# Kernel tuning notes

Measured on AMD Instinct MI355X. Metric: run time of the kernel, lower is better.

## Reference

```python
import jax, jax.numpy as jnp
import numpy as np

WORLD_SIZE = 8
BS = 16
MSG = 16384


def setup_inputs() -> dict:
    key = jax.random.key(0)
    k0, k1, kw, kb = jax.random.split(key, 4)
    x0 = jax.random.normal(k0, (WORLD_SIZE, BS, MSG), dtype=jnp.float32)
    x1 = jax.random.normal(k1, (WORLD_SIZE, BS, MSG), dtype=jnp.float32)
    # nn.Linear(msg_size, msg_size) params, kaiming-uniform-ish scale
    scale = 1.0 / np.sqrt(MSG)
    W = jax.random.uniform(kw, (MSG, MSG), dtype=jnp.float32, minval=-scale, maxval=scale)
    b = jax.random.uniform(kb, (MSG,), dtype=jnp.float32, minval=-scale, maxval=scale)
    return {"x0": x0, "x1": x1, "W": W, "b": b}


def reference(x0, x1, W, b):
    # all_gather_ll: concat per-rank shards along dim 0 -> [world_size*bs, msg]
    t0 = x0.reshape(WORLD_SIZE * BS, MSG)
    t1 = x1.reshape(WORLD_SIZE * BS, MSG)
    # shared Linear applied to both gathered tensors: y = t @ W^T + b
    y0 = jnp.einsum("nk,mk->nm", t0, W) + b
    y1 = jnp.einsum("nk,mk->nm", t1, W) + b
    return (y0, y1)
```

## Files before the change

### kernel.cpp

```cpp
#include <hip/hip_runtime.h>
#include <hip/hip_bf16.h>

typedef __bf16 bf16x8 __attribute__((ext_vector_type(8)));
typedef float  f32x4  __attribute__((ext_vector_type(4)));

#define N_TOT   16384
#define K_TOT   16384
#define HALF_M  ((size_t)128 * 16384)
#define BN      128
#define BK      32
#define KSPLIT  4
#define KQ_LEN  (K_TOT / KSPLIT)
#define NQSTEPS (KQ_LEN / BK)
#define OUT_ELEMS ((size_t)256 * 16384)

__device__ __forceinline__ unsigned short f2bf(float f) {
    __hip_bfloat16 h = __float2bfloat16(f);
    return __builtin_bit_cast(unsigned short, h);
}

__device__ __forceinline__ int swz64(int row, int g) {
    return row * 64 + (((g ^ ((row >> 1) & 3)) & 3) << 4);
}

__global__ void cvtT_kernel(const float* __restrict__ x0,
                            const float* __restrict__ x1,
                            unsigned short* __restrict__ wsT) {
    size_t i = (size_t)blockIdx.x * blockDim.x + threadIdx.x;
    size_t e = i * 8;
    const float* src = (e < HALF_M) ? (x0 + e) : (x1 + (e - HALF_M));
    float4 a = ((const float4*)src)[0];
    float4 b = ((const float4*)src)[1];
    union { unsigned short u[8]; uint4 v; } o;
    o.u[0] = f2bf(a.x); o.u[1] = f2bf(a.y); o.u[2] = f2bf(a.z); o.u[3] = f2bf(a.w);
    o.u[4] = f2bf(b.x); o.u[5] = f2bf(b.y); o.u[6] = f2bf(b.z); o.u[7] = f2bf(b.w);
    ((uint4*)wsT)[i] = o.v;
}

__global__ void combine_kernel(float* __restrict__ out,
                               const float* __restrict__ p0,
                               const float* __restrict__ p1,
                               const float* __restrict__ p2) {
    const size_t n4 = OUT_ELEMS / 4;
    size_t i = (size_t)blockIdx.x * blockDim.x + threadIdx.x;
    for (; i < n4; i += (size_t)gridDim.x * blockDim.x) {
        float4 o = ((const float4*)out)[i];
        float4 a = ((const float4*)p0)[i];
        float4 b = ((const float4*)p1)[i];
        float4 c = ((const float4*)p2)[i];
        o.x += a.x + b.x + c.x;  o.y += a.y + b.y + c.y;
        o.z += a.z + b.z + c.z;  o.w += a.w + b.w + c.w;
        ((float4*)out)[i] = o;
    }
}

#define ISSUEW(S, k0) do {                                                    \
    const uint4* _p = (const uint4*)(arow_w + (k0));                          \
    w##S##_0 = _p[0]; w##S##_1 = _p[1];                                       \
    const float4* _q = (const float4*)(brow + (k0));                          \
    wb##S##_0 = _q[0]; wb##S##_1 = _q[1];                                     \
} while (0)

#define STAGEW(S, Ab, Bb) do {                                                \
    *(uint4*)((Ab) + aw0) = w##S##_0;                                         \
    *(uint4*)((Ab) + aw1) = w##S##_1;                                         \
    union { unsigned short u[8]; uint4 v; } _tb;                              \
    _tb.u[0]=f2bf(wb##S##_0.x); _tb.u[1]=f2bf(wb##S##_0.y);                   \
    _tb.u[2]=f2bf(wb##S##_0.z); _tb.u[3]=f2bf(wb##S##_0.w);                   \
    _tb.u[4]=f2bf(wb##S##_1.x); _tb.u[5]=f2bf(wb##S##_1.y);                   \
    _tb.u[6]=f2bf(wb##S##_1.z); _tb.u[7]=f2bf(wb##S##_1.w);                   \
    *(uint4*)((Bb) + bw) = _tb.v;                                             \
} while (0)

#define COMPUTE(Ab, Bb) do {                                                  \
    bf16x8 _vb0 = *(const bf16x8*)((Bb) + boff0);                             \
    bf16x8 _vb1 = *(const bf16x8*)((Bb) + boff0 + 1024);                      \
    bf16x8 _va;                                                               \
    _va = *(const bf16x8*)((Ab) + aoff0 + 0*1024);                            \
    accA0 = __builtin_amdgcn_mfma_f32_16x16x32_bf16(_va, _vb0, accA0, 0,0,0); \
    accB0 = __builtin_amdgcn_mfma_f32_16x16x32_bf16(_va, _vb1, accB0, 0,0,0); \
    _va = *(const bf16x8*)((Ab) + aoff0 + 1*1024);                            \
    accA1 = __builtin_amdgcn_mfma_f32_16x16x32_bf16(_va, _vb0, accA1, 0,0,0); \
    accB1 = __builtin_amdgcn_mfma_f32_16x16x32_bf16(_va, _vb1, accB1, 0,0,0); \
    _va = *(const bf16x8*)((Ab) + aoff0 + 2*1024);                            \
    accA2 = __builtin_amdgcn_mfma_f32_16x16x32_bf16(_va, _vb0, accA2, 0,0,0); \
    accB2 = __builtin_amdgcn_mfma_f32_16x16x32_bf16(_va, _vb1, accB2, 0,0,0); \
    _va = *(const bf16x8*)((Ab) + aoff0 + 3*1024);                            \
    accA3 = __builtin_amdgcn_mfma_f32_16x16x32_bf16(_va, _vb0, accA3, 0,0,0); \
    accB3 = __builtin_amdgcn_mfma_f32_16x16x32_bf16(_va, _vb1, accB3, 0,0,0); \
    _va = *(const bf16x8*)((Ab) + aoff0 + 4*1024);                            \
    accA4 = __builtin_amdgcn_mfma_f32_16x16x32_bf16(_va, _vb0, accA4, 0,0,0); \
    accB4 = __builtin_amdgcn_mfma_f32_16x16x32_bf16(_va, _vb1, accB4, 0,0,0); \
    _va = *(const bf16x8*)((Ab) + aoff0 + 5*1024);                            \
    accA5 = __builtin_amdgcn_mfma_f32_16x16x32_bf16(_va, _vb0, accA5, 0,0,0); \
    accB5 = __builtin_amdgcn_mfma_f32_16x16x32_bf16(_va, _vb1, accB5, 0,0,0); \
    _va = *(const bf16x8*)((Ab) + aoff0 + 6*1024);                            \
    accA6 = __builtin_amdgcn_mfma_f32_16x16x32_bf16(_va, _vb0, accA6, 0,0,0); \
    accB6 = __builtin_amdgcn_mfma_f32_16x16x32_bf16(_va, _vb1, accB6, 0,0,0); \
    _va = *(const bf16x8*)((Ab) + aoff0 + 7*1024);                            \
    accA7 = __builtin_amdgcn_mfma_f32_16x16x32_bf16(_va, _vb0, accA7, 0,0,0); \
    accB7 = __builtin_amdgcn_mfma_f32_16x16x32_bf16(_va, _vb1, accB7, 0,0,0); \
} while (0)

#define SYNC do {                                                             \
    asm volatile("s_waitcnt lgkmcnt(0)" ::: "memory");                        \
    __builtin_amdgcn_s_barrier();                                             \
    __builtin_amdgcn_sched_barrier(0);                                        \
} while (0)

__global__ __launch_bounds__(512, 4)
void gemm_ws(const float* __restrict__ W, const float* __restrict__ bias,
             const unsigned short* __restrict__ wsT,
             float* __restrict__ out, float* __restrict__ wsP)
{
    __shared__ uint4 smem_[(2 * 16384 + 2 * 8192) / 16];
    char* const sm = (char*)smem_;
    char* const A0 = sm;
    char* const A1 = sm + 16384;
    char* const B0 = sm + 32768;
    char* const B1 = sm + 32768 + 8192;

    const int tid  = threadIdx.x;
    const int lane = tid & 63;
    const int wave = tid >> 6;
    const int wm = wave >> 2;
    const int wn = wave & 3;
    const int bid    = blockIdx.x;
    const int kq     = bid >> 7;
    const int nstrip = bid & 127;
    const int n0     = nstrip * BN;
    const int kbase  = kq * KQ_LEN;

    const int ra = tid >> 1;
    const int pa = tid & 1;
    const int rb = tid >> 2;
    const int gb = tid & 3;

    const unsigned short* arow_w = wsT + (size_t)ra * K_TOT + kbase + pa * 16;
    const float* brow = W + (size_t)(n0 + rb) * K_TOT + kbase + gb * 8;

    const int aw0 = swz64(ra, 2 * pa);
    const int aw1 = swz64(ra, 2 * pa + 1);
    const int bw  = swz64(rb, gb);

    const int aoff0 = swz64(wm * 128 + (lane & 15), lane >> 4);
    const int boff0 = swz64(wn * 32 + (lane & 15), lane >> 4);

    f32x4 accA0={0.f,0.f,0.f,0.f}, accA1={0.f,0.f,0.f,0.f};
    f32x4 accA2={0.f,0.f,0.f,0.f}, accA3={0.f,0.f,0.f,0.f};
    f32x4 accA4={0.f,0.f,0.f,0.f}, accA5={0.f,0.f,0.f,0.f};
    f32x4 accA6={0.f,0.f,0.f,0.f}, accA7={0.f,0.f,0.f,0.f};
    f32x4 accB0={0.f,0.f,0.f,0.f}, accB1={0.f,0.f,0.f,0.f};
    f32x4 accB2={0.f,0.f,0.f,0.f}, accB3={0.f,0.f,0.f,0.f};
    f32x4 accB4={0.f,0.f,0.f,0.f}, accB5={0.f,0.f,0.f,0.f};
    f32x4 accB6={0.f,0.f,0.f,0.f}, accB7={0.f,0.f,0.f,0.f};

    uint4  w0_0, w0_1, w1_0, w1_1;
    float4 wb0_0, wb0_1, wb1_0, wb1_1;

    ISSUEW(0, 0);
    ISSUEW(1, BK);
    STAGEW(0, A0, B0);
    SYNC;

    for (int kt = 0; kt < NQSTEPS; kt += 2) {
        if (kt + 2 < NQSTEPS) ISSUEW(0, (kt + 2) * BK);
        COMPUTE(A0, B0);
        STAGEW(1, A1, B1);
        SYNC;
        if (kt + 3 < NQSTEPS) ISSUEW(1, (kt + 3) * BK);
        COMPUTE(A1, B1);
        if (kt + 2 < NQSTEPS) STAGEW(0, A0, B0);
        SYNC;
    }

    float* const dst = (kq == 0) ? out : (wsP + (size_t)(kq - 1) * OUT_ELEMS);
    #pragma unroll
    for (int nf = 0; nf < 2; ++nf) {
        const int col = n0 + wn * 32 + nf * 16 + (lane & 15);
        const float bv = (kq == 0) ? bias[col] : 0.f;
        #pragma unroll
        for (int mf = 0; mf < 8; ++mf) {
            const f32x4 a = (nf == 0)
                ? (mf==0?accA0:mf==1?accA1:mf==2?accA2:mf==3?accA3:
                   mf==4?accA4:mf==5?accA5:mf==6?accA6:accA7)
                : (mf==0?accB0:mf==1?accB1:mf==2?accB2:mf==3?accB3:
                   mf==4?accB4:mf==5?accB5:mf==6?accB6:accB7);
            #pragma unroll
            for (int j = 0; j < 4; ++j) {
                int r = wm * 128 + mf * 16 + (lane >> 4) * 4 + j;
                float v = a[j] + bv;
                float* o = (r < 128) ? (dst + (size_t)r * N_TOT + col)
                                     : (dst + HALF_M + (size_t)(r - 128) * N_TOT + col);
                *o = v;
            }
        }
    }
}

extern "C" void kernel_launch(void* const* d_in, const int* in_sizes, int n_in,
                              void* d_out, int out_size, void* d_ws, size_t ws_size,
                              hipStream_t stream) {
    const float* x0 = (const float*)d_in[0];
    const float* x1 = (const float*)d_in[1];
    const float* W  = (const float*)d_in[2];
    const float* b  = (const float*)d_in[3];
    float* out = (float*)d_out;

    const size_t wsT_bytes = (size_t)256 * 16384 * sizeof(unsigned short);

    unsigned short* wsT = (unsigned short*)d_ws;
    float* wsP = (float*)((char*)d_ws + wsT_bytes);

    cvtT_kernel<<<2048, 256, 0, stream>>>(x0, x1, wsT);
    gemm_ws<<<512, 512, 0, stream>>>(W, b, wsT, out, wsP);
    combine_kernel<<<2048, 256, 0, stream>>>(out, wsP, wsP + OUT_ELEMS,
                                             wsP + 2 * OUT_ELEMS);
}
```

Baseline: 322.6 us.

## Load W fragments straight to registers and let each wave cover all 256 rows

The GEMM block shrinks from 512 to 256 threads. Each of the 4 waves now owns a 32-column N slice and all 256 activation rows, so it holds 32 accumulator tiles. W is no longer staged through LDS: each lane loads its own fp32 W fragment from global memory, converts it to bf16 in registers and feeds it directly to MFMA. Only the activation tile stays in double-buffered LDS. This removes the LDS writes, reads and bank traffic for W and halves the LDS footprint, at the cost of much higher register pressure and lower occupancy. W global loads are also less coalesced per lane, since each lane reads a 32-byte chunk from a different row.

```diff
diff --git a/kernel.cpp b/kernel.cpp
--- a/kernel.cpp
+++ b/kernel.cpp
@@ -54,52 +54,51 @@
     }
 }
 
-#define ISSUEW(S, k0) do {                                                    \
-    const uint4* _p = (const uint4*)(arow_w + (k0));                          \
-    w##S##_0 = _p[0]; w##S##_1 = _p[1];                                       \
-    const float4* _q = (const float4*)(brow + (k0));                          \
-    wb##S##_0 = _q[0]; wb##S##_1 = _q[1];                                     \
-} while (0)
-
-#define STAGEW(S, Ab, Bb) do {                                                \
-    *(uint4*)((Ab) + aw0) = w##S##_0;                                         \
-    *(uint4*)((Ab) + aw1) = w##S##_1;                                         \
-    union { unsigned short u[8]; uint4 v; } _tb;                              \
-    _tb.u[0]=f2bf(wb##S##_0.x); _tb.u[1]=f2bf(wb##S##_0.y);                   \
-    _tb.u[2]=f2bf(wb##S##_0.z); _tb.u[3]=f2bf(wb##S##_0.w);                   \
-    _tb.u[4]=f2bf(wb##S##_1.x); _tb.u[5]=f2bf(wb##S##_1.y);                   \
-    _tb.u[6]=f2bf(wb##S##_1.z); _tb.u[7]=f2bf(wb##S##_1.w);                   \
-    *(uint4*)((Bb) + bw) = _tb.v;                                             \
-} while (0)
-
-#define COMPUTE(Ab, Bb) do {                                                  \
-    bf16x8 _vb0 = *(const bf16x8*)((Bb) + boff0);                             \
-    bf16x8 _vb1 = *(const bf16x8*)((Bb) + boff0 + 1024);                      \
-    bf16x8 _va;                                                               \
-    _va = *(const bf16x8*)((Ab) + aoff0 + 0*1024);                            \
-    accA0 = __builtin_amdgcn_mfma_f32_16x16x32_bf16(_va, _vb0, accA0, 0,0,0); \
-    accB0 = __builtin_amdgcn_mfma_f32_16x16x32_bf16(_va, _vb1, accB0, 0,0,0); \
-    _va = *(const bf16x8*)((Ab) + aoff0 + 1*1024);                            \
-    accA1 = __builtin_amdgcn_mfma_f32_16x16x32_bf16(_va, _vb0, accA1, 0,0,0); \
-    accB1 = __builtin_amdgcn_mfma_f32_16x16x32_bf16(_va, _vb1, accB1, 0,0,0); \
-    _va = *(const bf16x8*)((Ab) + aoff0 + 2*1024);                            \
-    accA2 = __builtin_amdgcn_mfma_f32_16x16x32_bf16(_va, _vb0, accA2, 0,0,0); \
-    accB2 = __builtin_amdgcn_mfma_f32_16x16x32_bf16(_va, _vb1, accB2, 0,0,0); \
-    _va = *(const bf16x8*)((Ab) + aoff0 + 3*1024);                            \
-    accA3 = __builtin_amdgcn_mfma_f32_16x16x32_bf16(_va, _vb0, accA3, 0,0,0); \
-    accB3 = __builtin_amdgcn_mfma_f32_16x16x32_bf16(_va, _vb1, accB3, 0,0,0); \
-    _va = *(const bf16x8*)((Ab) + aoff0 + 4*1024);                            \
-    accA4 = __builtin_amdgcn_mfma_f32_16x16x32_bf16(_va, _vb0, accA4, 0,0,0); \
-    accB4 = __builtin_amdgcn_mfma_f32_16x16x32_bf16(_va, _vb1, accB4, 0,0,0); \
-    _va = *(const bf16x8*)((Ab) + aoff0 + 5*1024);                            \
-    accA5 = __builtin_amdgcn_mfma_f32_16x16x32_bf16(_va, _vb0, accA5, 0,0,0); \
-    accB5 = __builtin_amdgcn_mfma_f32_16x16x32_bf16(_va, _vb1, accB5, 0,0,0); \
-    _va = *(const bf16x8*)((Ab) + aoff0 + 6*1024);                            \
-    accA6 = __builtin_amdgcn_mfma_f32_16x16x32_bf16(_va, _vb0, accA6, 0,0,0); \
-    accB6 = __builtin_amdgcn_mfma_f32_16x16x32_bf16(_va, _vb1, accB6, 0,0,0); \
-    _va = *(const bf16x8*)((Ab) + aoff0 + 7*1024);                            \
-    accA7 = __builtin_amdgcn_mfma_f32_16x16x32_bf16(_va, _vb0, accA7, 0,0,0); \
-    accB7 = __builtin_amdgcn_mfma_f32_16x16x32_bf16(_va, _vb1, accB7, 0,0,0); \
+#define ISSUE_A(S, kt) do {                                                   \
+    const uint4* _p = (const uint4*)(arow + (size_t)(kt) * BK);               \
+    a##S##_0 = _p[0]; a##S##_1 = _p[1]; a##S##_2 = _p[2]; a##S##_3 = _p[3];   \
+} while (0)
+
+#define STAGE_A(S, Ab) do {                                                   \
+    *(uint4*)((Ab) + sw0) = a##S##_0;                                         \
+    *(uint4*)((Ab) + sw1) = a##S##_1;                                         \
+    *(uint4*)((Ab) + sw2) = a##S##_2;                                         \
+    *(uint4*)((Ab) + sw3) = a##S##_3;                                         \
+} while (0)
+
+#define ISSUE_W(S, kt) do {                                                   \
+    const float4* _q0 = (const float4*)(wrow0 + (size_t)(kt) * BK);           \
+    w##S##_a0 = _q0[0]; w##S##_a1 = _q0[1];                                   \
+    const float4* _q1 = (const float4*)(wrow1 + (size_t)(kt) * BK);           \
+    w##S##_b0 = _q1[0]; w##S##_b1 = _q1[1];                                   \
+} while (0)
+
+#define CVT_W(S) do {                                                         \
+    union { unsigned short u[8]; bf16x8 v; } _c0, _c1;                        \
+    _c0.u[0]=f2bf(w##S##_a0.x); _c0.u[1]=f2bf(w##S##_a0.y);                   \
+    _c0.u[2]=f2bf(w##S##_a0.z); _c0.u[3]=f2bf(w##S##_a0.w);                   \
+    _c0.u[4]=f2bf(w##S##_a1.x); _c0.u[5]=f2bf(w##S##_a1.y);                   \
+    _c0.u[6]=f2bf(w##S##_a1.z); _c0.u[7]=f2bf(w##S##_a1.w);                   \
+    _c1.u[0]=f2bf(w##S##_b0.x); _c1.u[1]=f2bf(w##S##_b0.y);                   \
+    _c1.u[2]=f2bf(w##S##_b0.z); _c1.u[3]=f2bf(w##S##_b0.w);                   \
+    _c1.u[4]=f2bf(w##S##_b1.x); _c1.u[5]=f2bf(w##S##_b1.y);                   \
+    _c1.u[6]=f2bf(w##S##_b1.z); _c1.u[7]=f2bf(w##S##_b1.w);                   \
+    _vb0 = _c0.v; _vb1 = _c1.v;                                               \
+} while (0)
+
+#define MROW(MF, Ab) do {                                                     \
+    bf16x8 _va = *(const bf16x8*)((Ab) + aoff0 + MF * 1024);                  \
+    accA##MF = __builtin_amdgcn_mfma_f32_16x16x32_bf16(_va, _vb0, accA##MF, 0,0,0); \
+    accB##MF = __builtin_amdgcn_mfma_f32_16x16x32_bf16(_va, _vb1, accB##MF, 0,0,0); \
+} while (0)
+
+#define COMPUTE(Ab, S) do {                                                   \
+    bf16x8 _vb0, _vb1;                                                        \
+    CVT_W(S);                                                                 \
+    MROW(0, Ab);  MROW(1, Ab);  MROW(2, Ab);  MROW(3, Ab);                    \
+    MROW(4, Ab);  MROW(5, Ab);  MROW(6, Ab);  MROW(7, Ab);                    \
+    MROW(8, Ab);  MROW(9, Ab);  MROW(10, Ab); MROW(11, Ab);                   \
+    MROW(12, Ab); MROW(13, Ab); MROW(14, Ab); MROW(15, Ab);                   \
 } while (0)
 
 #define SYNC do {                                                             \
@@ -108,87 +107,90 @@
     __builtin_amdgcn_sched_barrier(0);                                        \
 } while (0)
 
-__global__ __launch_bounds__(512, 4)
+__global__ __launch_bounds__(256)
 void gemm_ws(const float* __restrict__ W, const float* __restrict__ bias,
              const unsigned short* __restrict__ wsT,
              float* __restrict__ out, float* __restrict__ wsP)
 {
-    __shared__ uint4 smem_[(2 * 16384 + 2 * 8192) / 16];
+    __shared__ uint4 smem_[2 * 16384 / 16];
     char* const sm = (char*)smem_;
     char* const A0 = sm;
     char* const A1 = sm + 16384;
-    char* const B0 = sm + 32768;
-    char* const B1 = sm + 32768 + 8192;
 
     const int tid  = threadIdx.x;
     const int lane = tid & 63;
     const int wave = tid >> 6;
-    const int wm = wave >> 2;
-    const int wn = wave & 3;
     const int bid    = blockIdx.x;
     const int kq     = bid >> 7;
     const int nstrip = bid & 127;
     const int n0     = nstrip * BN;
     const int kbase  = kq * KQ_LEN;
 
-    const int ra = tid >> 1;
-    const int pa = tid & 1;
-    const int rb = tid >> 2;
-    const int gb = tid & 3;
-
-    const unsigned short* arow_w = wsT + (size_t)ra * K_TOT + kbase + pa * 16;
-    const float* brow = W + (size_t)(n0 + rb) * K_TOT + kbase + gb * 8;
-
-    const int aw0 = swz64(ra, 2 * pa);
-    const int aw1 = swz64(ra, 2 * pa + 1);
-    const int bw  = swz64(rb, gb);
-
-    const int aoff0 = swz64(wm * 128 + (lane & 15), lane >> 4);
-    const int boff0 = swz64(wn * 32 + (lane & 15), lane >> 4);
-
-    f32x4 accA0={0.f,0.f,0.f,0.f}, accA1={0.f,0.f,0.f,0.f};
-    f32x4 accA2={0.f,0.f,0.f,0.f}, accA3={0.f,0.f,0.f,0.f};
-    f32x4 accA4={0.f,0.f,0.f,0.f}, accA5={0.f,0.f,0.f,0.f};
-    f32x4 accA6={0.f,0.f,0.f,0.f}, accA7={0.f,0.f,0.f,0.f};
-    f32x4 accB0={0.f,0.f,0.f,0.f}, accB1={0.f,0.f,0.f,0.f};
-    f32x4 accB2={0.f,0.f,0.f,0.f}, accB3={0.f,0.f,0.f,0.f};
-    f32x4 accB4={0.f,0.f,0.f,0.f}, accB5={0.f,0.f,0.f,0.f};
-    f32x4 accB6={0.f,0.f,0.f,0.f}, accB7={0.f,0.f,0.f,0.f};
-
-    uint4  w0_0, w0_1, w1_0, w1_1;
-    float4 wb0_0, wb0_1, wb1_0, wb1_1;
-
-    ISSUEW(0, 0);
-    ISSUEW(1, BK);
-    STAGEW(0, A0, B0);
+    const unsigned short* arow = wsT + (size_t)tid * K_TOT + kbase;
+    const int sw0 = swz64(tid, 0);
+    const int sw1 = swz64(tid, 1);
+    const int sw2 = swz64(tid, 2);
+    const int sw3 = swz64(tid, 3);
+
+    const int nrow0 = n0 + wave * 32 + (lane & 15);
+    const float* wrow0 = W + (size_t)nrow0 * K_TOT + kbase + (lane >> 4) * 8;
+    const float* wrow1 = wrow0 + (size_t)16 * K_TOT;
+
+    const int aoff0 = swz64(lane & 15, lane >> 4);
+
+    f32x4 accA0={0,0,0,0}, accA1={0,0,0,0}, accA2={0,0,0,0}, accA3={0,0,0,0};
+    f32x4 accA4={0,0,0,0}, accA5={0,0,0,0}, accA6={0,0,0,0}, accA7={0,0,0,0};
+    f32x4 accA8={0,0,0,0}, accA9={0,0,0,0}, accA10={0,0,0,0}, accA11={0,0,0,0};
+    f32x4 accA12={0,0,0,0}, accA13={0,0,0,0}, accA14={0,0,0,0}, accA15={0,0,0,0};
+    f32x4 accB0={0,0,0,0}, accB1={0,0,0,0}, accB2={0,0,0,0}, accB3={0,0,0,0};
+    f32x4 accB4={0,0,0,0}, accB5={0,0,0,0}, accB6={0,0,0,0}, accB7={0,0,0,0};
+    f32x4 accB8={0,0,0,0}, accB9={0,0,0,0}, accB10={0,0,0,0}, accB11={0,0,0,0};
+    f32x4 accB12={0,0,0,0}, accB13={0,0,0,0}, accB14={0,0,0,0}, accB15={0,0,0,0};
+
+    uint4  a0_0, a0_1, a0_2, a0_3, a1_0, a1_1, a1_2, a1_3;
+    float4 w0_a0, w0_a1, w0_b0, w0_b1, w1_a0, w1_a1, w1_b0, w1_b1;
+
+    ISSUE_A(0, 0); ISSUE_W(0, 0);
+    ISSUE_A(1, 1); ISSUE_W(1, 1);
+    STAGE_A(0, A0);
     SYNC;
 
     for (int kt = 0; kt < NQSTEPS; kt += 2) {
-        if (kt + 2 < NQSTEPS) ISSUEW(0, (kt + 2) * BK);
-        COMPUTE(A0, B0);
-        STAGEW(1, A1, B1);
-        SYNC;
-        if (kt + 3 < NQSTEPS) ISSUEW(1, (kt + 3) * BK);
-        COMPUTE(A1, B1);
-        if (kt + 2 < NQSTEPS) STAGEW(0, A0, B0);
-        SYNC;
+        {
+            const bool more = (kt + 2 < NQSTEPS);
+            COMPUTE(A0, 0);
+            if (more) { ISSUE_W(0, kt + 2); ISSUE_A(0, kt + 2); }
+            STAGE_A(1, A1);
+            SYNC;
+        }
+        {
+            const bool more = (kt + 3 < NQSTEPS);
+            COMPUTE(A1, 1);
+            if (more) { ISSUE_W(1, kt + 3); ISSUE_A(1, kt + 3); }
+            if (kt + 2 < NQSTEPS) STAGE_A(0, A0);
+            SYNC;
+        }
     }
 
     float* const dst = (kq == 0) ? out : (wsP + (size_t)(kq - 1) * OUT_ELEMS);
     #pragma unroll
     for (int nf = 0; nf < 2; ++nf) {
-        const int col = n0 + wn * 32 + nf * 16 + (lane & 15);
+        const int col = n0 + wave * 32 + nf * 16 + (lane & 15);
         const float bv = (kq == 0) ? bias[col] : 0.f;
         #pragma unroll
-        for (int mf = 0; mf < 8; ++mf) {
+        for (int mf = 0; mf < 16; ++mf) {
             const f32x4 a = (nf == 0)
                 ? (mf==0?accA0:mf==1?accA1:mf==2?accA2:mf==3?accA3:
-                   mf==4?accA4:mf==5?accA5:mf==6?accA6:accA7)
+                   mf==4?accA4:mf==5?accA5:mf==6?accA6:mf==7?accA7:
+                   mf==8?accA8:mf==9?accA9:mf==10?accA10:mf==11?accA11:
+                   mf==12?accA12:mf==13?accA13:mf==14?accA14:accA15)
                 : (mf==0?accB0:mf==1?accB1:mf==2?accB2:mf==3?accB3:
-                   mf==4?accB4:mf==5?accB5:mf==6?accB6:accB7);
+                   mf==4?accB4:mf==5?accB5:mf==6?accB6:mf==7?accB7:
+                   mf==8?accB8:mf==9?accB9:mf==10?accB10:mf==11?accB11:
+                   mf==12?accB12:mf==13?accB13:mf==14?accB14:accB15);
             #pragma unroll
             for (int j = 0; j < 4; ++j) {
-                int r = wm * 128 + mf * 16 + (lane >> 4) * 4 + j;
+                int r = mf * 16 + (lane >> 4) * 4 + j;
                 float v = a[j] + bv;
                 float* o = (r < 128) ? (dst + (size_t)r * N_TOT + col)
                                      : (dst + HALF_M + (size_t)(r - 128) * N_TOT + col);
@@ -213,7 +215,7 @@
     float* wsP = (float*)((char*)d_ws + wsT_bytes);
 
     cvtT_kernel<<<2048, 256, 0, stream>>>(x0, x1, wsT);
-    gemm_ws<<<512, 512, 0, stream>>>(W, b, wsT, out, wsP);
+    gemm_ws<<<512, 256, 0, stream>>>(W, b, wsT, out, wsP);
     combine_kernel<<<2048, 256, 0, stream>>>(out, wsP, wsP + OUT_ELEMS,
                                              wsP + 2 * OUT_ELEMS);
 }
```

New measurement: 500.5 us. +55.1%, slower.
